# Kernel tuning notes

Hardware: AMD Instinct MI355X
Metric: run time of the kernel (lower is better)

Reference implementation:

```python
import jax, jax.numpy as jnp
import numpy as np

D_MODEL = 2048
HEADS = 16
HEAD_DIM = D_MODEL // HEADS  # 128


def setup_inputs() -> dict:
    key = jax.random.key(0)
    k1, k2, k3 = jax.random.split(key, 3)
    B, S = 1, 2048
    x = jax.random.normal(k1, (B, S, D_MODEL), dtype=jnp.float32)
    Wqkv_w = jax.random.normal(k2, (D_MODEL + 2 * HEAD_DIM, D_MODEL), dtype=jnp.float32) * (D_MODEL ** -0.5)
    Wqkv_b = jnp.zeros((D_MODEL + 2 * HEAD_DIM,), dtype=jnp.float32)
    out_w = jax.random.normal(k3, (D_MODEL, D_MODEL), dtype=jnp.float32) * (D_MODEL ** -0.5)
    out_b = jnp.zeros((D_MODEL,), dtype=jnp.float32)
    return {"x": x, "Wqkv_w": Wqkv_w, "Wqkv_b": Wqkv_b, "out_w": out_w, "out_b": out_b}


def reference(x, Wqkv_w, Wqkv_b, out_w, out_b):
    B, S, _ = x.shape
    # fused QKV projection
    qkv = jnp.einsum('bsd,ed->bse', x, Wqkv_w) + Wqkv_b  # [B,S,D+2*hd]
    q = qkv[..., :D_MODEL]                               # [B,S,D]
    k = qkv[..., D_MODEL:D_MODEL + HEAD_DIM]             # [B,S,hd] single KV head
    v = qkv[..., D_MODEL + HEAD_DIM:]                    # [B,S,hd]
    q = q.reshape(B, S, HEADS, HEAD_DIM)                 # [B,S,H,hd]
    scale = 1.0 / np.sqrt(HEAD_DIM)
    # QK^T with shared K head, scaled
    scores = jnp.einsum('bqhd,bkd->bhqk', q, k) * scale  # [B,H,S,S]
    # causal mask (additive fill with dtype min, matching masked_fill)
    min_val = jnp.finfo(scores.dtype).min
    causal = jnp.tril(jnp.ones((S, S), dtype=bool))
    scores = jnp.where(causal[None, None], scores, min_val)
    attn = jax.nn.softmax(scores, axis=-1)               # [B,H,S,S]
    ctx = jnp.einsum('bhqk,bkd->bqhd', attn, v)          # [B,S,H,hd]
    ctx = ctx.reshape(B, S, D_MODEL)
    out = jnp.einsum('bsd,ed->bse', ctx, out_w) + out_b  # [B,S,D]
    return out
```

## Files before the change

kernel.cpp:

```cpp
#include <hip/hip_runtime.h>
#include <hip/hip_bf16.h>
#include <math.h>


#define S_LEN 2048
#define DMODEL 2048
#define EQKV 2304
#define HDIM 128
#define NHEADS 16
#define VTS 2080

typedef _Float16 f16;
typedef __attribute__((ext_vector_type(8))) _Float16 f16x8;
typedef __attribute__((ext_vector_type(4))) _Float16 f16x4;
typedef __attribute__((ext_vector_type(4))) float f32x4;

#define MFMA16(a, b, c) __builtin_amdgcn_mfma_f32_16x16x32_f16((a), (b), (c), 0, 0, 0)

#define ALPHA 0.12751879526655967f
#define CFIX 10.0f

__device__ __forceinline__ void load_lds16(const void* g, void* l) {
  __builtin_amdgcn_global_load_lds((const __attribute__((address_space(1))) void*)g,
                                   (__attribute__((address_space(3))) void*)l, 16, 0, 0);
}

__global__ void cast3_kernel(const float* __restrict__ a, const float* __restrict__ b,
                             const float* __restrict__ c, f16* __restrict__ dst) {
  int i = blockIdx.x * blockDim.x + threadIdx.x;
  const float* src;
  int off;
  if (i < 1048576) { src = a; off = 0; }
  else if (i < 1048576 + 1179648) { src = b; off = 1048576; }
  else { src = c; off = 1048576 + 1179648; }
  float4 v = reinterpret_cast<const float4*>(src)[i - off];
  f16x4 o = {(f16)v.x, (f16)v.y, (f16)v.z, (f16)v.w};
  reinterpret_cast<f16x4*>(dst)[i] = o;
}

__device__ __forceinline__ void gemm_stage(const f16* __restrict__ A,
                                           const f16* __restrict__ Bm,
                                           int bm, int bn, int K, int k0,
                                           char* base, int w, int l) {
#pragma unroll
  for (int i = 0; i < 2; ++i) {
    int slot = i * 256 + w * 64 + l;
    int row = slot >> 3;
    int cg = (slot & 7) ^ (row & 7);
    load_lds16(A + (size_t)(bm * 64 + row) * K + k0 + cg * 8,
               base + (i * 256 + w * 64) * 16);
  }
#pragma unroll
  for (int i = 0; i < 4; ++i) {
    int slot = i * 256 + w * 64 + l;
    int row = slot >> 3;
    int cg = (slot & 7) ^ (row & 7);
    load_lds16(Bm + (size_t)(bn * 128 + row) * K + k0 + cg * 8,
               base + 8192 + (i * 256 + w * 64) * 16);
  }
}

template <typename OutT, bool QKV>
__global__ __launch_bounds__(256) void gemm_bt(
    const f16* __restrict__ A, const f16* __restrict__ Bm,
    const float* __restrict__ bias, OutT* __restrict__ C,
    f16* __restrict__ VT, int M, int N, int K) {
  __shared__ __align__(16) char smem[49152];
  const int tid = threadIdx.x;
  const int w = tid >> 6;
  const int l = tid & 63;
  const int bm = blockIdx.x, bn = blockIdx.y;
  const int wm = w >> 1, wn = w & 1;
  const int lg = l >> 4;
  const int lm = l & 15;
  const int l7 = l & 7;

  f32x4 acc[2][4] = {};

  int aoff[2][2], boff[4][2];
#pragma unroll
  for (int mf = 0; mf < 2; ++mf) {
    int row = wm * 32 + mf * 16 + lm;
#pragma unroll
    for (int kk = 0; kk < 2; ++kk)
      aoff[mf][kk] = row * 128 + ((kk * 4 + lg) ^ l7) * 16;
  }
#pragma unroll
  for (int nf = 0; nf < 4; ++nf) {
    int row = wn * 64 + nf * 16 + lm;
#pragma unroll
    for (int kk = 0; kk < 2; ++kk)
      boff[nf][kk] = 8192 + row * 128 + ((kk * 4 + lg) ^ l7) * 16;
  }

  const int nkt = K >> 6;
  gemm_stage(A, Bm, bm, bn, K, 0, smem, w, l);
  __syncthreads();
  int buf = 0;
  for (int kt = 0; kt < nkt; ++kt) {
    char* cur = smem + buf * 24576;
    if (kt + 1 < nkt)
      gemm_stage(A, Bm, bm, bn, K, (kt + 1) << 6, smem + (buf ^ 1) * 24576, w, l);
#pragma unroll
    for (int kk = 0; kk < 2; ++kk) {
      f16x8 af[2], bf[4];
#pragma unroll
      for (int mf = 0; mf < 2; ++mf)
        af[mf] = *reinterpret_cast<const f16x8*>(cur + aoff[mf][kk]);
#pragma unroll
      for (int nf = 0; nf < 4; ++nf)
        bf[nf] = *reinterpret_cast<const f16x8*>(cur + boff[nf][kk]);
#pragma unroll
      for (int mf = 0; mf < 2; ++mf)
#pragma unroll
        for (int nf = 0; nf < 4; ++nf)
          acc[mf][nf] = MFMA16(af[mf], bf[nf], acc[mf][nf]);
    }
    __syncthreads();
    buf ^= 1;
  }

#pragma unroll
  for (int mf = 0; mf < 2; ++mf) {
#pragma unroll
    for (int nf = 0; nf < 4; ++nf) {
      int col = bn * 128 + wn * 64 + nf * 16 + lm;
      float bv = bias[col];
#pragma unroll
      for (int j = 0; j < 4; ++j) {
        int row = bm * 64 + wm * 32 + mf * 16 + lg * 4 + j;
        float v = acc[mf][nf][j] + bv;
        if (QKV && col >= DMODEL + HDIM) {
          VT[(size_t)(col - DMODEL - HDIM) * VTS + row] = (f16)v;
        } else {
          C[(size_t)row * N + col] = (OutT)v;
        }
      }
    }
  }
}

__device__ __forceinline__ void stage_kv(const f16* __restrict__ qkv,
                                         const f16* __restrict__ vt, int k0,
                                         char* kb, char* vb, int tid, int wv) {
#pragma unroll
  for (int i = 0; i < 4; ++i) {
    int slot = i * 256 + tid;
    int r = slot >> 4;
    int cs = (slot & 15) ^ (r & 7);
    load_lds16(qkv + (size_t)(k0 + r) * EQKV + DMODEL + cs * 8,
               kb + (i * 256 + wv * 64) * 16);
  }
#pragma unroll
  for (int i = 0; i < 4; ++i) {
    int slot = i * 256 + tid;
    int d = slot >> 3;
    int cs = (slot & 7) ^ (d & 7);
    load_lds16(vt + (size_t)d * VTS + k0 + cs * 8,
               vb + (i * 256 + wv * 64) * 16);
  }
}

__global__ __launch_bounds__(256, 2) void flash_mha4(
    const f16* __restrict__ qkv, const f16* __restrict__ vt, f16* __restrict__ ctx,
    f16* __restrict__ Opart, float* __restrict__ lbuf) {
  const int qt32 = blockIdx.x;
  const int ch = blockIdx.y;
  const int hg = blockIdx.z;
  const int ktiles = (qt32 >> 1) + 1;
  if (ch * 8 >= ktiles) return;

  extern __shared__ char smem[];
  const int tid = threadIdx.x;
  const int wv = tid >> 6;
  const int l = tid & 63;
  const int lg = l >> 4, lm = l & 15;
  char* Pb = smem + 65536 + wv * 4096;
  const int head = hg * 4 + wv;
  const int wq0 = qt32 * 32;

  f16x8 qf[2][4];
#pragma unroll
  for (int mf = 0; mf < 2; ++mf)
#pragma unroll
    for (int ks = 0; ks < 4; ++ks)
      qf[mf][ks] = *reinterpret_cast<const f16x8*>(
          qkv + (size_t)(wq0 + mf * 16 + lm) * EQKV + head * HDIM + ks * 32 + lg * 8);

  f32x4 o[2][8] = {};
  float lsum[2][4] = {};

  const int kt0 = ch * 8;
  const int kt1 = min(ktiles, kt0 + 8);

  stage_kv(qkv, vt, kt0 * 64, smem, smem + 32768, tid, wv);
  int buf = 0;

  for (int t = kt0; t < kt1; ++t) {
    __syncthreads();
    char* kb = smem + buf * 16384;
    char* vb = smem + 32768 + buf * 16384;
    if (t + 1 < kt1)
      stage_kv(qkv, vt, (t + 1) * 64, smem + (buf ^ 1) * 16384,
               smem + 32768 + (buf ^ 1) * 16384, tid, wv);
    const int k0 = t * 64;

    f32x4 sc[2][4] = {};
#pragma unroll
    for (int ks = 0; ks < 4; ++ks) {
#pragma unroll
      for (int nf = 0; nf < 4; ++nf) {
        int row = nf * 16 + lm;
        int pos = (ks * 4 + lg) ^ (row & 7);
        f16x8 kf = *reinterpret_cast<const f16x8*>(kb + row * 256 + pos * 16);
        sc[0][nf] = MFMA16(qf[0][ks], kf, sc[0][nf]);
        sc[1][nf] = MFMA16(qf[1][ks], kf, sc[1][nf]);
      }
    }
    if (t == ktiles - 1) {
#pragma unroll
      for (int mf = 0; mf < 2; ++mf)
#pragma unroll
        for (int nf = 0; nf < 4; ++nf)
#pragma unroll
          for (int j = 0; j < 4; ++j) {
            int row = wq0 + mf * 16 + lg * 4 + j;
            int col = k0 + nf * 16 + lm;
            if (col > row) sc[mf][nf][j] = -__builtin_inff();
          }
    }
#pragma unroll
    for (int mf = 0; mf < 2; ++mf)
#pragma unroll
      for (int nf = 0; nf < 4; ++nf)
#pragma unroll
        for (int j = 0; j < 4; ++j) {
          float p = exp2f(sc[mf][nf][j] * ALPHA - CFIX);
          lsum[mf][j] += p;
          int prow = mf * 16 + lg * 4 + j;
          int c = nf * 2 + (lm >> 3);
          *reinterpret_cast<f16*>(Pb + prow * 128 + ((c ^ (prow & 7)) * 16 + (lm & 7) * 2)) = (f16)p;
        }
    asm volatile("s_waitcnt lgkmcnt(0)" ::: "memory");
    __builtin_amdgcn_sched_barrier(0);
#pragma unroll
    for (int kk = 0; kk < 2; ++kk) {
      f16x8 pa[2];
#pragma unroll
      for (int mf = 0; mf < 2; ++mf) {
        int prow = mf * 16 + lm;
        int pos = (kk * 4 + lg) ^ (prow & 7);
        pa[mf] = *reinterpret_cast<const f16x8*>(Pb + prow * 128 + pos * 16);
      }
#pragma unroll
      for (int df = 0; df < 8; ++df) {
        int d = df * 16 + lm;
        int pos = (kk * 4 + lg) ^ (d & 7);
        f16x8 vf = *reinterpret_cast<const f16x8*>(vb + d * 128 + pos * 16);
        o[0][df] = MFMA16(pa[0], vf, o[0][df]);
        o[1][df] = MFMA16(pa[1], vf, o[1][df]);
      }
    }
    buf ^= 1;
  }

#pragma unroll
  for (int mf = 0; mf < 2; ++mf)
#pragma unroll
    for (int j = 0; j < 4; ++j) {
#pragma unroll
      for (int d = 1; d < 16; d <<= 1) lsum[mf][j] += __shfl_xor(lsum[mf][j], d);
    }

  if (qt32 < 16) {
#pragma unroll
    for (int mf = 0; mf < 2; ++mf)
#pragma unroll
      for (int j = 0; j < 4; ++j) {
        float inv = 1.0f / lsum[mf][j];
        int row = wq0 + mf * 16 + lg * 4 + j;
#pragma unroll
        for (int df = 0; df < 8; ++df)
          ctx[(size_t)row * DMODEL + head * HDIM + df * 16 + lm] =
              (f16)(o[mf][df][j] * inv);
      }
  } else {
    const int slot = head * 192 + (qt32 - 16) * 4 + ch;
    f16* Op = Opart + (size_t)slot * 4096;
    float* lp = lbuf + (size_t)slot * 32;
#pragma unroll
    for (int mf = 0; mf < 2; ++mf)
#pragma unroll
      for (int j = 0; j < 4; ++j) {
        int rl = mf * 16 + lg * 4 + j;
#pragma unroll
        for (int df = 0; df < 8; ++df)
          Op[rl * 128 + df * 16 + lm] = (f16)o[mf][df][j];
        if (lm == 0) lp[rl] = lsum[mf][j];
      }
  }
}

__global__ __launch_bounds__(128) void flash_combine(
    const f16* __restrict__ Opart, const float* __restrict__ lbuf,
    f16* __restrict__ ctx) {
  const int qt32 = blockIdx.x, head = blockIdx.y;
  if (qt32 < 16) return;
  const int ktiles = (qt32 >> 1) + 1;
  const int nch = (ktiles + 7) >> 3;
  const int tid = threadIdx.x;
  const int row = tid >> 2, cg = tid & 3;
  const int slot0 = head * 192 + (qt32 - 16) * 4;

  float L = 0.f;
  for (int i = 0; i < nch; ++i) L += lbuf[(size_t)(slot0 + i) * 32 + row];
  const float invL = 1.0f / L;
  const int rowg = qt32 * 32 + row;

#pragma unroll
  for (int g = 0; g < 4; ++g) {
    float acc[8] = {0.f, 0.f, 0.f, 0.f, 0.f, 0.f, 0.f, 0.f};
    for (int i = 0; i < nch; ++i) {
      f16x8 v = *reinterpret_cast<const f16x8*>(
          Opart + (size_t)(slot0 + i) * 4096 + row * 128 + cg * 32 + g * 8);
#pragma unroll
      for (int j = 0; j < 8; ++j) acc[j] += (float)v[j];
    }
    f16x8 ov;
#pragma unroll
    for (int j = 0; j < 8; ++j) ov[j] = (f16)(acc[j] * invL);
    *reinterpret_cast<f16x8*>(ctx + (size_t)rowg * DMODEL + head * HDIM + cg * 32 + g * 8) = ov;
  }
}

extern "C" void kernel_launch(void* const* d_in, const int* in_sizes, int n_in,
                              void* d_out, int out_size, void* d_ws, size_t ws_size,
                              hipStream_t stream) {
  const float* x = (const float*)d_in[0];
  const float* Wqkv_w = (const float*)d_in[1];
  const float* Wqkv_b = (const float*)d_in[2];
  const float* out_w = (const float*)d_in[3];
  const float* out_b = (const float*)d_in[4];

  char* p = (char*)d_ws;
  f16* xh = (f16*)p;    p += (size_t)S_LEN * DMODEL * 2;
  f16* wqh = (f16*)p;   p += (size_t)EQKV * DMODEL * 2;
  f16* owh = (f16*)p;   p += (size_t)DMODEL * DMODEL * 2;
  f16* qkvh = (f16*)p;  p += (size_t)S_LEN * EQKV * 2;
  f16* vth = (f16*)p;   p += (size_t)HDIM * VTS * 2;
  f16* ctxh = (f16*)p;  p += (size_t)S_LEN * DMODEL * 2;
  f16* Opart = (f16*)p;   p += (size_t)3072 * 4096 * 2;
  float* lbuf = (float*)p; p += (size_t)3072 * 32 * 4;

  cast3_kernel<<<12800, 256, 0, stream>>>(x, Wqkv_w, out_w, xh);

  gemm_bt<f16, true><<<dim3(S_LEN / 64, EQKV / 128), 256, 0, stream>>>(
      xh, wqh, Wqkv_b, qkvh, vth, S_LEN, EQKV, DMODEL);

  flash_mha4<<<dim3(64, 4, 4), 256, 81920, stream>>>(qkvh, vth, ctxh, Opart, lbuf);
  flash_combine<<<dim3(64, 16), 128, 0, stream>>>(Opart, lbuf, ctxh);

  gemm_bt<float, false><<<dim3(S_LEN / 64, DMODEL / 128), 256, 0, stream>>>(
      ctxh, owh, out_b, (float*)d_out, nullptr, S_LEN, DMODEL, DMODEL);
}
```

Measured before the change: 211.5 us.

## Enlarge GEMM tiles to 128x128 with triple-buffered LDS pipeline and XCD swizzle

Both projection GEMMs now use 128x128 output tiles instead of 64x128, doubling per-wave MFMA work and operand reuse. The LDS pipeline moves from double to triple buffering with explicit vmcnt waits and raw barriers, so loads run two stages ahead. A 1-D grid with an XCD-aware block remap places neighbouring tiles on the same chiplet to improve L2 reuse. The cost is fewer blocks (288/256, about one wave on the device), 96KB dynamic LDS per block limiting occupancy, and hand-tuned waitcnt counts that must match the number of issued loads.

```diff
diff --git a/kernel.cpp b/kernel.cpp
--- a/kernel.cpp
+++ b/kernel.cpp
@@ -40,23 +40,23 @@
 
 __device__ __forceinline__ void gemm_stage(const f16* __restrict__ A,
                                            const f16* __restrict__ Bm,
-                                           int bm, int bn, int K, int k0,
+                                           int arow0, int brow0, int K, int k0,
                                            char* base, int w, int l) {
-#pragma unroll
-  for (int i = 0; i < 2; ++i) {
-    int slot = i * 256 + w * 64 + l;
-    int row = slot >> 3;
-    int cg = (slot & 7) ^ (row & 7);
-    load_lds16(A + (size_t)(bm * 64 + row) * K + k0 + cg * 8,
-               base + (i * 256 + w * 64) * 16);
-  }
 #pragma unroll
   for (int i = 0; i < 4; ++i) {
     int slot = i * 256 + w * 64 + l;
     int row = slot >> 3;
     int cg = (slot & 7) ^ (row & 7);
-    load_lds16(Bm + (size_t)(bn * 128 + row) * K + k0 + cg * 8,
-               base + 8192 + (i * 256 + w * 64) * 16);
+    load_lds16(A + (size_t)(arow0 + row) * K + k0 + cg * 8,
+               base + (i * 256 + w * 64) * 16);
+  }
+#pragma unroll
+  for (int i = 0; i < 4; ++i) {
+    int slot = i * 256 + w * 64 + l;
+    int row = slot >> 3;
+    int cg = (slot & 7) ^ (row & 7);
+    load_lds16(Bm + (size_t)(brow0 + row) * K + k0 + cg * 8,
+               base + 16384 + (i * 256 + w * 64) * 16);
   }
 }
 
@@ -64,23 +64,23 @@
 __global__ __launch_bounds__(256) void gemm_bt(
     const f16* __restrict__ A, const f16* __restrict__ Bm,
     const float* __restrict__ bias, OutT* __restrict__ C,
-    f16* __restrict__ VT, int M, int N, int K) {
-  __shared__ __align__(16) char smem[49152];
+    f16* __restrict__ VT, int NBN, int N, int K) {
+  extern __shared__ char smem[];
+  const int cpx = gridDim.x >> 3;
+  const int wg = (blockIdx.x & 7) * cpx + (blockIdx.x >> 3);
+  const int bm = wg / NBN, bn = wg % NBN;
+
   const int tid = threadIdx.x;
-  const int w = tid >> 6;
-  const int l = tid & 63;
-  const int bm = blockIdx.x, bn = blockIdx.y;
+  const int w = tid >> 6, l = tid & 63;
   const int wm = w >> 1, wn = w & 1;
-  const int lg = l >> 4;
-  const int lm = l & 15;
-  const int l7 = l & 7;
-
-  f32x4 acc[2][4] = {};
-
-  int aoff[2][2], boff[4][2];
-#pragma unroll
-  for (int mf = 0; mf < 2; ++mf) {
-    int row = wm * 32 + mf * 16 + lm;
+  const int lg = l >> 4, lm = l & 15, l7 = l & 7;
+
+  f32x4 acc[4][4] = {};
+
+  int aoff[4][2], boff[4][2];
+#pragma unroll
+  for (int mf = 0; mf < 4; ++mf) {
+    int row = wm * 64 + mf * 16 + lm;
 #pragma unroll
     for (int kk = 0; kk < 2; ++kk)
       aoff[mf][kk] = row * 128 + ((kk * 4 + lg) ^ l7) * 16;
@@ -90,45 +90,57 @@
     int row = wn * 64 + nf * 16 + lm;
 #pragma unroll
     for (int kk = 0; kk < 2; ++kk)
-      boff[nf][kk] = 8192 + row * 128 + ((kk * 4 + lg) ^ l7) * 16;
-  }
-
+      boff[nf][kk] = 16384 + row * 128 + ((kk * 4 + lg) ^ l7) * 16;
+  }
+
+  const int arow0 = bm * 128, brow0 = bn * 128;
   const int nkt = K >> 6;
-  gemm_stage(A, Bm, bm, bn, K, 0, smem, w, l);
-  __syncthreads();
-  int buf = 0;
-  for (int kt = 0; kt < nkt; ++kt) {
-    char* cur = smem + buf * 24576;
-    if (kt + 1 < nkt)
-      gemm_stage(A, Bm, bm, bn, K, (kt + 1) << 6, smem + (buf ^ 1) * 24576, w, l);
+
+  gemm_stage(A, Bm, arow0, brow0, K, 0, smem, w, l);
+  gemm_stage(A, Bm, arow0, brow0, K, 64, smem + 32768, w, l);
+
+  int rb = 0;
+  for (int t = 0; t < nkt; ++t) {
+    __builtin_amdgcn_s_barrier();
+    if (t + 2 < nkt) {
+      int nb = rb + 2 >= 3 ? rb - 1 : rb + 2;
+      gemm_stage(A, Bm, arow0, brow0, K, (t + 2) << 6, smem + nb * 32768, w, l);
+      asm volatile("s_waitcnt vmcnt(16)" ::: "memory");
+    } else if (t + 1 < nkt) {
+      asm volatile("s_waitcnt vmcnt(8)" ::: "memory");
+    } else {
+      asm volatile("s_waitcnt vmcnt(0)" ::: "memory");
+    }
+    __builtin_amdgcn_sched_barrier(0);
+    __builtin_amdgcn_s_barrier();
+    char* cur = smem + rb * 32768;
 #pragma unroll
     for (int kk = 0; kk < 2; ++kk) {
-      f16x8 af[2], bf[4];
-#pragma unroll
-      for (int mf = 0; mf < 2; ++mf)
+      f16x8 af[4], bf[4];
+#pragma unroll
+      for (int mf = 0; mf < 4; ++mf)
         af[mf] = *reinterpret_cast<const f16x8*>(cur + aoff[mf][kk]);
 #pragma unroll
       for (int nf = 0; nf < 4; ++nf)
         bf[nf] = *reinterpret_cast<const f16x8*>(cur + boff[nf][kk]);
 #pragma unroll
-      for (int mf = 0; mf < 2; ++mf)
+      for (int mf = 0; mf < 4; ++mf)
 #pragma unroll
         for (int nf = 0; nf < 4; ++nf)
           acc[mf][nf] = MFMA16(af[mf], bf[nf], acc[mf][nf]);
     }
-    __syncthreads();
-    buf ^= 1;
-  }
-
-#pragma unroll
-  for (int mf = 0; mf < 2; ++mf) {
+    rb = rb + 1 >= 3 ? 0 : rb + 1;
+  }
+
+#pragma unroll
+  for (int mf = 0; mf < 4; ++mf) {
 #pragma unroll
     for (int nf = 0; nf < 4; ++nf) {
       int col = bn * 128 + wn * 64 + nf * 16 + lm;
       float bv = bias[col];
 #pragma unroll
       for (int j = 0; j < 4; ++j) {
-        int row = bm * 64 + wm * 32 + mf * 16 + lg * 4 + j;
+        int row = bm * 128 + wm * 64 + mf * 16 + lg * 4 + j;
         float v = acc[mf][nf][j] + bv;
         if (QKV && col >= DMODEL + HDIM) {
           VT[(size_t)(col - DMODEL - HDIM) * VTS + row] = (f16)v;
@@ -354,12 +366,12 @@
 
   cast3_kernel<<<12800, 256, 0, stream>>>(x, Wqkv_w, out_w, xh);
 
-  gemm_bt<f16, true><<<dim3(S_LEN / 64, EQKV / 128), 256, 0, stream>>>(
-      xh, wqh, Wqkv_b, qkvh, vth, S_LEN, EQKV, DMODEL);
+  gemm_bt<f16, true><<<288, 256, 98304, stream>>>(
+      xh, wqh, Wqkv_b, qkvh, vth, 18, EQKV, DMODEL);
 
   flash_mha4<<<dim3(64, 4, 4), 256, 81920, stream>>>(qkvh, vth, ctxh, Opart, lbuf);
   flash_combine<<<dim3(64, 16), 128, 0, stream>>>(Opart, lbuf, ctxh);
 
-  gemm_bt<float, false><<<dim3(S_LEN / 64, DMODEL / 128), 256, 0, stream>>>(
-      ctxh, owh, out_b, (float*)d_out, nullptr, S_LEN, DMODEL, DMODEL);
-}
+  gemm_bt<float, false><<<256, 256, 98304, stream>>>(
+      ctxh, owh, out_b, (float*)d_out, nullptr, 16, DMODEL, DMODEL);
+}
```

Measured after the change: 232.9 us. +10.1%, slower.
